# Kernel tuning notes

Measured on AMD Instinct MI355X. Metric: run time of the kernel, lower is better.

The kernel has to match this reference:

```python
import jax, jax.numpy as jnp
import numpy as np
import math

NEG_INF = -1e9
ALPHA = 1.0


def setup_inputs() -> dict:
    key = jax.random.key(0)
    B, T, S, C = 32, 1024, 512, 384
    k1, k2 = jax.random.split(key)
    epsilon = jax.random.normal(k1, (B, T, C), dtype=jnp.float32)
    conditional_inputs = jax.random.normal(k2, (B, S, C), dtype=jnp.float32)
    targets_lengths = jnp.full((B,), T, dtype=jnp.int32)
    condition_lengths = jnp.full((B,), S, dtype=jnp.int32)
    return {
        "epsilon": epsilon,
        "conditional_inputs": conditional_inputs,
        "targets_lengths": targets_lengths,
        "condition_lengths": condition_lengths,
    }


def _forward_dp(E):
    """Log-partition forward DP. E = alpha*Wr, [B,T,S].
    mu[t,j] = E[t,j] + logaddexp(mu[t-1,j], mu[t-1,j-1]); path starts at (0,0)."""
    B, T, S = E.shape
    start = jnp.where(jnp.arange(S) == 0, 0.0, NEG_INF)
    init = E[:, 0, :] + start[None, :]

    def step(mu_prev, e_t):
        shifted = jnp.concatenate([jnp.full((B, 1), NEG_INF, mu_prev.dtype), mu_prev[:, :-1]], axis=1)
        mu_t = e_t + jnp.logaddexp(mu_prev, shifted)
        return mu_t, mu_t

    _, mus = jax.lax.scan(step, init, jnp.moveaxis(E[:, 1:], 1, 0))
    return jnp.concatenate([init[:, None], jnp.moveaxis(mus, 0, 1)], axis=1)  # [B,T,S]


def _backward_dp(E):
    """Backward messages. beta[T-1,j] = 0 at j=S-1 else -inf;
    beta[t,j] = logaddexp(beta[t+1,j]+E[t+1,j], beta[t+1,j+1]+E[t+1,j+1])."""
    B, T, S = E.shape
    init = jnp.broadcast_to(jnp.where(jnp.arange(S) == S - 1, 0.0, NEG_INF), (B, S))

    def step(b_next, e_next):
        m = b_next + e_next
        shifted = jnp.concatenate([m[:, 1:], jnp.full((B, 1), NEG_INF, m.dtype)], axis=1)
        b_t = jnp.logaddexp(m, shifted)
        return b_t, b_t

    _, bs = jax.lax.scan(step, init, jnp.moveaxis(E[:, 1:], 1, 0), reverse=True)
    return jnp.concatenate([jnp.moveaxis(bs, 0, 1), init[:, None]], axis=1)  # [B,T,S]


def _maximum_path(logpi):
    """Viterbi over monotonic paths (stay at j or step to j from j-1 each t).
    Returns binary path [B,T,S]."""
    B, T, S = logpi.shape
    start = jnp.where(jnp.arange(S) == 0, 0.0, NEG_INF)
    init = logpi[:, 0, :] + start[None, :]

    def step(v_prev, lp_t):
        shifted = jnp.concatenate([jnp.full((B, 1), NEG_INF, v_prev.dtype), v_prev[:, :-1]], axis=1)
        v_t = lp_t + jnp.maximum(v_prev, shifted)
        move = shifted > v_prev  # True => predecessor is j-1
        return v_t, move

    _, moves = jax.lax.scan(step, init, jnp.moveaxis(logpi[:, 1:], 1, 0))  # [T-1,B,S]

    j_last = jnp.full((B,), S - 1, dtype=jnp.int32)

    def back(j, move_t):
        came = jnp.take_along_axis(move_t, j[:, None].astype(jnp.int32), axis=1)[:, 0]
        j_prev = j - came.astype(jnp.int32)
        return j_prev, j

    j0, js = jax.lax.scan(back, j_last, moves, reverse=True)  # js[i] = j at time i+1
    js_all = jnp.concatenate([j0[None], js], axis=0)  # [T,B]
    return jax.nn.one_hot(jnp.moveaxis(js_all, 0, 1), S, dtype=logpi.dtype)  # [B,T,S]


def reference(epsilon, conditional_inputs, targets_lengths, condition_lengths):
    B, T, C = epsilon.shape
    S = conditional_inputs.shape[1]
    # initial gaussian sample log-prob, masked by target lengths
    logp_eps = -0.5 * (epsilon ** 2 + math.log(2.0 * math.pi))
    tmask = (jnp.arange(T)[None, :] < targets_lengths[:, None]).astype(epsilon.dtype)
    logprobs = jnp.sum(tmask[:, :, None] * logp_eps, axis=(1, 2))

    z = epsilon  # Glow is external; treated as identity flow (logdet = 0)

    # score matrix + softmax over the target axis (dim 1), as in the source
    Wr = jnp.einsum("btc,bsc->bts", z, conditional_inputs)
    Wr = jax.nn.softmax(Wr, axis=1)

    E = ALPHA * Wr
    mu = _forward_dp(E)
    mu_N = mu[:, -1, -1]
    beta = _backward_dp(E)
    logpi = mu + beta - mu_N[:, None, None]  # posterior node log-marginals

    path = _maximum_path(logpi)  # [B,T,S] binary alignment
    sample_logprob = ALPHA * jnp.sum(path * Wr, axis=(1, 2)) - mu_N
    logprobs = logprobs + sample_logprob
    return path, logprobs
```

## Files before the change

### kernel.cpp

```cpp
#include <hip/hip_runtime.h>
#include <cstdint>
#include <cstddef>

#define B_ 32
#define T_ 1024
#define S_ 512
#define C_ 384
#define HALF_LOG_2PI 0.91893853320467274178f
#define LN2F 0.69314718055994530942f
#define INV_LN2F 1.44269504088896340736f

typedef unsigned short u16;
typedef unsigned long long u64;
typedef __attribute__((ext_vector_type(8))) short bf16x8;
typedef __attribute__((ext_vector_type(4))) float f32x4;

__device__ __forceinline__ unsigned rne16(float f) {
    unsigned b = __float_as_uint(f);
    return (b + 0x7FFFu + ((b >> 16) & 1u)) >> 16;
}
__device__ __forceinline__ uint4 pack8f(float a0, float a1, float a2, float a3,
                                        float a4, float a5, float a6, float a7) {
    uint4 q;
    q.x = rne16(a0) | (rne16(a1) << 16);
    q.y = rne16(a2) | (rne16(a3) << 16);
    q.z = rne16(a4) | (rne16(a5) << 16);
    q.w = rne16(a6) | (rne16(a7) << 16);
    return q;
}
#define UNPK(q, p)                                                              \
    float p##0 = __uint_as_float((q).x << 16),                                  \
          p##1 = __uint_as_float((q).x & 0xFFFF0000u),                          \
          p##2 = __uint_as_float((q).y << 16),                                  \
          p##3 = __uint_as_float((q).y & 0xFFFF0000u),                          \
          p##4 = __uint_as_float((q).z << 16),                                  \
          p##5 = __uint_as_float((q).z & 0xFFFF0000u),                          \
          p##6 = __uint_as_float((q).w << 16),                                  \
          p##7 = __uint_as_float((q).w & 0xFFFF0000u)

#define PROW(t) (*(const uint4*)(Pb  + (size_t)(t) * S_ + l8))
#define BROW(t) (*(const uint4*)(Btb + (size_t)(t) * S_ + l8))

template <int CTRL>
__device__ __forceinline__ float fdpp0(float x) {
    return __uint_as_float((unsigned)__builtin_amdgcn_update_dpp(
        0, (int)__float_as_uint(x), CTRL, 0xF, 0xF, true));
}
__device__ __forceinline__ float wave_fmax(float x) {
    x = fmaxf(x, fdpp0<0x121>(x));
    x = fmaxf(x, fdpp0<0x122>(x));
    x = fmaxf(x, fdpp0<0x124>(x));
    x = fmaxf(x, fdpp0<0x128>(x));
    float a = __uint_as_float((unsigned)__builtin_amdgcn_readlane((int)__float_as_uint(x), 0));
    float b = __uint_as_float((unsigned)__builtin_amdgcn_readlane((int)__float_as_uint(x), 16));
    float c = __uint_as_float((unsigned)__builtin_amdgcn_readlane((int)__float_as_uint(x), 32));
    float d = __uint_as_float((unsigned)__builtin_amdgcn_readlane((int)__float_as_uint(x), 48));
    return fmaxf(fmaxf(a, b), fmaxf(c, d));
}

__device__ __forceinline__ void gll16(const u16* g, u16* l) {
    __builtin_amdgcn_global_load_lds(
        (const __attribute__((address_space(1))) void*)g,
        (__attribute__((address_space(3))) void*)l, 16, 0, 0);
}
#define WAITV(N) do { asm volatile("s_waitcnt vmcnt(" #N ")" ::: "memory");     \
                      __builtin_amdgcn_sched_barrier(0); } while (0)
#define FENCE_LGKM() do { asm volatile("s_waitcnt lgkmcnt(0)" ::: "memory");    \
                          __builtin_amdgcn_sched_barrier(0); } while (0)

__global__ __launch_bounds__(256) void k_pre(const float* __restrict__ eps,
                                             const float* __restrict__ cond,
                                             const int* __restrict__ tlen,
                                             float* __restrict__ lp_part,
                                             u16* __restrict__ Abf,
                                             u16* __restrict__ Bbf) {
    if (blockIdx.x < 1536) {
        const int b = blockIdx.x / 48, chunk = blockIdx.x % 48;
        const int len = tlen[b];
        const float* base = eps + (size_t)b * T_ * C_ + (size_t)chunk * 8192;
        u16* obase = Abf + (size_t)b * T_ * C_ + (size_t)chunk * 8192;
        float acc = 0.f;
        for (int g = threadIdx.x; g < 1024; g += 256) {
            float4 v0 = *(const float4*)(base + g * 8);
            float4 v1 = *(const float4*)(base + g * 8 + 4);
            int t = (chunk * 8192 + g * 8) / C_;
            if (t < len)
                acc += v0.x*v0.x + v0.y*v0.y + v0.z*v0.z + v0.w*v0.w
                     + v1.x*v1.x + v1.y*v1.y + v1.z*v1.z + v1.w*v1.w;
            *(uint4*)(obase + g * 8) = pack8f(v0.x, v0.y, v0.z, v0.w,
                                              v1.x, v1.y, v1.z, v1.w);
        }
        __shared__ float red[256];
        red[threadIdx.x] = acc;
        __syncthreads();
        for (int o = 128; o > 0; o >>= 1) {
            if (threadIdx.x < o) red[threadIdx.x] += red[threadIdx.x + o];
            __syncthreads();
        }
        if (threadIdx.x == 0) lp_part[blockIdx.x] = -0.5f * red[0];
    } else {
        const size_t n8 = (size_t)B_ * S_ * C_ / 8;
        for (size_t i = (size_t)(blockIdx.x - 1536) * 256 + threadIdx.x; i < n8;
             i += (size_t)512 * 256) {
            float4 v0 = *(const float4*)(cond + i * 8);
            float4 v1 = *(const float4*)(cond + i * 8 + 4);
            *(uint4*)(Bbf + i * 8) = pack8f(v0.x, v0.y, v0.z, v0.w,
                                            v1.x, v1.y, v1.z, v1.w);
        }
    }
}

__global__ __launch_bounds__(256) void k_gemm(const u16* __restrict__ A,
                                              const u16* __restrict__ Bc,
                                              u16* __restrict__ Wb) {
    __shared__ u16 Al[4096];
    __shared__ u16 Bl[4096];
    const int b  = blockIdx.z;
    const int m0 = blockIdx.y * 128;
    const int n0 = blockIdx.x * 128;
    const int tid = threadIdx.x;
    const int lane = tid & 63, wid = tid >> 6;
    const int wy = wid >> 1, wx = wid & 1;
    const int r15 = lane & 15, kg = lane >> 4;
    const u16* Ab = A  + (size_t)b * T_ * C_;
    const u16* Bb = Bc + (size_t)b * S_ * C_;

    f32x4 acc[4][4];
#pragma unroll
    for (int i = 0; i < 4; ++i)
#pragma unroll
        for (int j = 0; j < 4; ++j) acc[i][j] = (f32x4){0.f, 0.f, 0.f, 0.f};

    const int g1 = tid + 256;
    const int row0 = tid >> 2, o0 = tid & 3;
    const int row1 = g1 >> 2,  o1 = g1 & 3;
    const int wb0 = (row0 * 64 + o0 * 16) ^ (((row0 >> 1) & 7) << 4);
    const int wb1 = (row1 * 64 + o1 * 16) ^ (((row1 >> 1) & 7) << 4);
    const int rswz = ((r15 >> 1) & 7) << 4;

    for (int k0 = 0; k0 < C_; k0 += 32) {
        uint4 a0 = *(const uint4*)(Ab + (size_t)(m0 + row0) * C_ + k0 + o0 * 8);
        uint4 a1 = *(const uint4*)(Ab + (size_t)(m0 + row1) * C_ + k0 + o1 * 8);
        uint4 c0 = *(const uint4*)(Bb + (size_t)(n0 + row0) * C_ + k0 + o0 * 8);
        uint4 c1 = *(const uint4*)(Bb + (size_t)(n0 + row1) * C_ + k0 + o1 * 8);
        __syncthreads();
        *(uint4*)((char*)Al + wb0) = a0;
        *(uint4*)((char*)Al + wb1) = a1;
        *(uint4*)((char*)Bl + wb0) = c0;
        *(uint4*)((char*)Bl + wb1) = c1;
        __syncthreads();
        bf16x8 af[4], bfb[4];
#pragma unroll
        for (int ar = 0; ar < 4; ++ar) {
            int row = wy * 64 + ar * 16 + r15;
            af[ar] = *(const bf16x8*)((const char*)Al + ((row * 64 + kg * 16) ^ rswz));
        }
#pragma unroll
        for (int bc = 0; bc < 4; ++bc) {
            int row = wx * 64 + bc * 16 + r15;
            bfb[bc] = *(const bf16x8*)((const char*)Bl + ((row * 64 + kg * 16) ^ rswz));
        }
#pragma unroll
        for (int ar = 0; ar < 4; ++ar)
#pragma unroll
            for (int bc = 0; bc < 4; ++bc)
                acc[ar][bc] = __builtin_amdgcn_mfma_f32_16x16x32_bf16(
                    af[ar], bfb[bc], acc[ar][bc], 0, 0, 0);
    }
#pragma unroll
    for (int ar = 0; ar < 4; ++ar) {
        int t = m0 + wy * 64 + ar * 16 + kg * 4;
#pragma unroll
        for (int bc = 0; bc < 4; ++bc) {
            int s = n0 + wx * 64 + bc * 16 + r15;
            u16* dst = Wb + ((size_t)b * T_ + t) * S_ + s;
#pragma unroll
            for (int r = 0; r < 4; ++r) dst[(size_t)r * S_] = (u16)rne16(acc[ar][bc][r]);
        }
    }
}

#define COLU(i, xa, xb, xc, xd) do {                                            \
    float nm = fmaxf(fmaxf(fmaxf(m[i], xa), xb), fmaxf(xc, xd));                \
    s[i] = s[i] * __builtin_amdgcn_exp2f((m[i] - nm) * INV_LN2F)                \
         + __builtin_amdgcn_exp2f((xa - nm) * INV_LN2F)                         \
         + __builtin_amdgcn_exp2f((xb - nm) * INV_LN2F)                         \
         + __builtin_amdgcn_exp2f((xc - nm) * INV_LN2F)                         \
         + __builtin_amdgcn_exp2f((xd - nm) * INV_LN2F);                        \
    m[i] = nm;                                                                  \
} while (0)

__global__ __launch_bounds__(256) void k_stats1(const u16* __restrict__ Wb,
                                                float* __restrict__ pmax,
                                                float* __restrict__ psum) {
    __shared__ float smax[4][S_];
    __shared__ float ssum[4][S_];
    const int c = blockIdx.x & 3;
    const int b = blockIdx.x >> 2;
    const int w = threadIdx.x >> 6, l = threadIdx.x & 63;
    const u16* base = Wb + (size_t)b * T_ * S_ + (size_t)(c * 256 + w * 64) * S_ + l * 8;
    float m[8], s[8];
#pragma unroll
    for (int i = 0; i < 8; ++i) { m[i] = -3.0e38f; s[i] = 0.f; }
    for (int t = 0; t < 64; t += 4) {
        uint4 q0 = *(const uint4*)(base + (size_t)(t + 0) * S_);
        uint4 q1 = *(const uint4*)(base + (size_t)(t + 1) * S_);
        uint4 q2 = *(const uint4*)(base + (size_t)(t + 2) * S_);
        uint4 q3 = *(const uint4*)(base + (size_t)(t + 3) * S_);
        UNPK(q0, xa); UNPK(q1, xb); UNPK(q2, xc); UNPK(q3, xd);
        COLU(0, xa0, xb0, xc0, xd0);
        COLU(1, xa1, xb1, xc1, xd1);
        COLU(2, xa2, xb2, xc2, xd2);
        COLU(3, xa3, xb3, xc3, xd3);
        COLU(4, xa4, xb4, xc4, xd4);
        COLU(5, xa5, xb5, xc5, xd5);
        COLU(6, xa6, xb6, xc6, xd6);
        COLU(7, xa7, xb7, xc7, xd7);
    }
#pragma unroll
    for (int i = 0; i < 8; ++i) {
        smax[w][l * 8 + i] = m[i];
        ssum[w][l * 8 + i] = s[i];
    }
    __syncthreads();
    for (int col = threadIdx.x; col < S_; col += 256) {
        float m0 = smax[0][col], m1 = smax[1][col];
        float m2 = smax[2][col], m3 = smax[3][col];
        float nm = fmaxf(fmaxf(m0, m1), fmaxf(m2, m3));
        float ss = ssum[0][col] * __builtin_amdgcn_exp2f((m0 - nm) * INV_LN2F)
                 + ssum[1][col] * __builtin_amdgcn_exp2f((m1 - nm) * INV_LN2F)
                 + ssum[2][col] * __builtin_amdgcn_exp2f((m2 - nm) * INV_LN2F)
                 + ssum[3][col] * __builtin_amdgcn_exp2f((m3 - nm) * INV_LN2F);
        pmax[(size_t)c * B_ * S_ + b * S_ + col] = nm;
        psum[(size_t)c * B_ * S_ + b * S_ + col] = ss;
    }
}

__global__ __launch_bounds__(256) void k_stats2(const float* __restrict__ pmax,
                                                const float* __restrict__ psum,
                                                float* __restrict__ cmax,
                                                float* __restrict__ cinv) {
    const int i = blockIdx.x * 256 + threadIdx.x;
    float m0 = pmax[i], m1 = pmax[(size_t)B_ * S_ + i];
    float m2 = pmax[(size_t)2 * B_ * S_ + i], m3 = pmax[(size_t)3 * B_ * S_ + i];
    float m = fmaxf(fmaxf(m0, m1), fmaxf(m2, m3));
    float s = psum[i] * expf(m0 - m)
            + psum[(size_t)B_ * S_ + i] * expf(m1 - m)
            + psum[(size_t)2 * B_ * S_ + i] * expf(m2 - m)
            + psum[(size_t)3 * B_ * S_ + i] * expf(m3 - m);
    cmax[i] = m;
    cinv[i] = 1.0f / s;
}

__global__ __launch_bounds__(256) void k_pack(const u16* __restrict__ Wb,
                                              const float* __restrict__ cmax,
                                              const float* __restrict__ cinv,
                                              u16* __restrict__ P) {
    const size_t total8 = (size_t)B_ * T_ * S_ / 8;
    for (size_t i = (size_t)blockIdx.x * 256 + threadIdx.x; i < total8;
         i += (size_t)gridDim.x * 256) {
        size_t base = i * 8;
        int s = (int)(base & (S_ - 1));
        int b = (int)(base >> 19);
        uint4 xq = *(const uint4*)(Wb + base);
        UNPK(xq, x);
        float4 mA = *(const float4*)(cmax + (size_t)b * S_ + s);
        float4 mB = *(const float4*)(cmax + (size_t)b * S_ + s + 4);
        float4 iA = *(const float4*)(cinv + (size_t)b * S_ + s);
        float4 iB = *(const float4*)(cinv + (size_t)b * S_ + s + 4);
        float w0 = __builtin_amdgcn_exp2f(fmaf(x0, INV_LN2F, -mA.x * INV_LN2F)) * iA.x;
        float w1 = __builtin_amdgcn_exp2f(fmaf(x1, INV_LN2F, -mA.y * INV_LN2F)) * iA.y;
        float w2 = __builtin_amdgcn_exp2f(fmaf(x2, INV_LN2F, -mA.z * INV_LN2F)) * iA.z;
        float w3 = __builtin_amdgcn_exp2f(fmaf(x3, INV_LN2F, -mA.w * INV_LN2F)) * iA.w;
        float w4 = __builtin_amdgcn_exp2f(fmaf(x4, INV_LN2F, -mB.x * INV_LN2F)) * iB.x;
        float w5 = __builtin_amdgcn_exp2f(fmaf(x5, INV_LN2F, -mB.y * INV_LN2F)) * iB.y;
        float w6 = __builtin_amdgcn_exp2f(fmaf(x6, INV_LN2F, -mB.z * INV_LN2F)) * iB.z;
        float w7 = __builtin_amdgcn_exp2f(fmaf(x7, INV_LN2F, -mB.w * INV_LN2F)) * iB.w;
        float p0 = __builtin_amdgcn_exp2f(fmaf(w0, INV_LN2F, -2.0f));
        float p1 = __builtin_amdgcn_exp2f(fmaf(w1, INV_LN2F, -2.0f));
        float p2 = __builtin_amdgcn_exp2f(fmaf(w2, INV_LN2F, -2.0f));
        float p3 = __builtin_amdgcn_exp2f(fmaf(w3, INV_LN2F, -2.0f));
        float p4 = __builtin_amdgcn_exp2f(fmaf(w4, INV_LN2F, -2.0f));
        float p5 = __builtin_amdgcn_exp2f(fmaf(w5, INV_LN2F, -2.0f));
        float p6 = __builtin_amdgcn_exp2f(fmaf(w6, INV_LN2F, -2.0f));
        float p7 = __builtin_amdgcn_exp2f(fmaf(w7, INV_LN2F, -2.0f));
        *(uint4*)(P + base) = pack8f(p0, p1, p2, p3, p4, p5, p6, p7);
    }
}

#define RENORM_B() do {                                                         \
    float mx_ = wave_fmax(fmaxf(fmaxf(fmaxf(m0,m1),fmaxf(m2,m3)),               \
                                fmaxf(fmaxf(m4,m5),fmaxf(m6,m7))));             \
    int eb_ = (__float_as_int(mx_) >> 23) & 255;                                \
    float sc_ = (eb_ > 0) ? __int_as_float((254 - eb_) << 23) : 1.0f;           \
    m0*=sc_; m1*=sc_; m2*=sc_; m3*=sc_; m4*=sc_; m5*=sc_; m6*=sc_; m7*=sc_;     \
} while (0)

#define BSTEPD(tt, jj) do {                                                     \
    uint4 q_ = *(const uint4*)&Pl[buf][jj][l8];                                 \
    UNPK(q_, eP);                                                               \
    float z0=m0*eP0, z1=m1*eP1, z2=m2*eP2, z3=m3*eP3;                           \
    float z4=m4*eP4, z5=m5*eP5, z6=m6*eP6, z7=m7*eP7;                           \
    float rt = fdpp0<0x130>(z0);                \
    m0=z0+z1; m1=z1+z2; m2=z2+z3; m3=z3+z4;                                     \
    m4=z4+z5; m5=z5+z6; m6=z6+z7; m7=z7+rt;                                     \
    if ((tt) < w0 + 32) {                                                       \
        uint4 st;                                                               \
        asm("v_cvt_pk_bf16_f32 %0, %1, %2" : "=v"(st.x) : "v"(m0), "v"(m1));    \
        asm("v_cvt_pk_bf16_f32 %0, %1, %2" : "=v"(st.y) : "v"(m2), "v"(m3));    \
        asm("v_cvt_pk_bf16_f32 %0, %1, %2" : "=v"(st.z) : "v"(m4), "v"(m5));    \
        asm("v_cvt_pk_bf16_f32 %0, %1, %2" : "=v"(st.w) : "v"(m6), "v"(m7));    \
        *(uint4*)(Bb + (size_t)(tt) * S_ + l8) = st;                            \
    }                                                                           \
} while (0)

__global__ __launch_bounds__(64) void k_beta(const u16* __restrict__ P,
                                             u16* __restrict__ Bt) {
    __shared__ u16 Pl[2][8][S_];
    const int l = threadIdx.x, l8 = l * 8;
    const int xcd = blockIdx.x & 7;
    const int idx = blockIdx.x >> 3;
    const int c = idx & 31;
    const int b = ((idx >> 5) << 3) + xcd;
    const int w0 = c * 32;
    const u16* Pb = P  + (size_t)b * T_ * S_;
    u16*      Bb = Bt + (size_t)b * T_ * S_;
    float m0, m1, m2, m3, m4, m5, m6, m7;
    int te = w0 + 63;
    if (te > 1023) te = 1023;
    if (te == 1023) {
        m0 = m1 = m2 = m3 = m4 = m5 = m6 = 0.f;
        m7 = (l == 63) ? 1.f : 0.f;
        if (1023 < w0 + 32) {
            uint4 st;
            asm("v_cvt_pk_bf16_f32 %0, %1, %2" : "=v"(st.x) : "v"(m0), "v"(m1));
            asm("v_cvt_pk_bf16_f32 %0, %1, %2" : "=v"(st.y) : "v"(m2), "v"(m3));
            asm("v_cvt_pk_bf16_f32 %0, %1, %2" : "=v"(st.z) : "v"(m4), "v"(m5));
            asm("v_cvt_pk_bf16_f32 %0, %1, %2" : "=v"(st.w) : "v"(m6), "v"(m7));
            *(uint4*)(Bb + (size_t)1023 * S_ + l8) = st;
        }
    } else {
        m0 = m1 = m2 = m3 = m4 = m5 = m6 = m7 = 1.f;
    }
    const int cnt = te - w0;
    const int ng = (cnt + 1) >> 3;
#pragma unroll
    for (int r = 0; r < 8; ++r)
        gll16(Pb + (size_t)(te - r) * S_ + l8, &Pl[0][r][0]);
#pragma unroll
    for (int r = 0; r < 8; ++r)
        gll16(Pb + (size_t)(te - 8 - r) * S_ + l8, &Pl[1][r][0]);
    int tt = te - 1;
    int buf = 0;
    for (int g = 0; g < ng - 1; ++g) {
        WAITV(8);
        BSTEPD(tt - 0, 0);  BSTEPD(tt - 1, 1);  BSTEPD(tt - 2, 2);  BSTEPD(tt - 3, 3);
        BSTEPD(tt - 4, 4);  BSTEPD(tt - 5, 5);  BSTEPD(tt - 6, 6);  BSTEPD(tt - 7, 7);
        RENORM_B();
        FENCE_LGKM();
        if (g + 2 < ng) {
            const int bs = te - 8 * (g + 2);
#pragma unroll
            for (int r = 0; r < 8; ++r)
                gll16(Pb + (size_t)(bs - r) * S_ + l8, &Pl[buf][r][0]);
        }
        __builtin_amdgcn_sched_barrier(0);
        buf ^= 1;
        tt -= 8;
    }
    WAITV(0);
    BSTEPD(tt - 0, 0);  BSTEPD(tt - 1, 1);  BSTEPD(tt - 2, 2);  BSTEPD(tt - 3, 3);
    BSTEPD(tt - 4, 4);  BSTEPD(tt - 5, 5);  BSTEPD(tt - 6, 6);
}

#define RENORM_MI() do {                                                        \
    float mx_ = wave_fmax(fmaxf(fmaxf(fmaxf(m0,m1),fmaxf(m2,m3)),               \
                                fmaxf(fmaxf(m4,m5),fmaxf(m6,m7))));             \
    int eb_ = (__float_as_int(mx_) >> 23) & 255;                                \
    float sc_ = (eb_ > 0) ? __int_as_float((254 - eb_) << 23) : 1.0f;           \
    if (eb_ > 0) ioffM += eb_ - 127;                                            \
    m0*=sc_; m1*=sc_; m2*=sc_; m3*=sc_; m4*=sc_; m5*=sc_; m6*=sc_; m7*=sc_;     \
} while (0)

#define RENORM_VR() do {                                                        \
    float mx_ = wave_fmax(fmaxf(fmaxf(fmaxf(v0,v1),fmaxf(v2,v3)),               \
                                fmaxf(fmaxf(v4,v5),fmaxf(v6,v7))));             \
    int eb_ = (__float_as_int(mx_) >> 23) & 255;                                \
    float sc_ = (eb_ > 0) ? __int_as_float((254 - eb_) << 23) : 0.0f;           \
    float ad_ = (eb_ > 0) ? 0.f : 1.f;                                          \
    v0=fmaf(v0,sc_,ad_); v1=fmaf(v1,sc_,ad_); v2=fmaf(v2,sc_,ad_);              \
    v3=fmaf(v3,sc_,ad_); v4=fmaf(v4,sc_,ad_); v5=fmaf(v5,sc_,ad_);              \
    v6=fmaf(v6,sc_,ad_); v7=fmaf(v7,sc_,ad_);                                   \
} while (0)

#define VSTEPD(TT, jj) do {                                                     \
    uint4 qp_ = *(const uint4*)&Pl[buf][jj][l8];                                \
    uint4 qb_ = *(const uint4*)&Bl[buf][jj][l8];                                \
    UNPK(qp_, eP); UNPK(qb_, eB);                                               \
    float lf = fdpp0<0x138>(m7);                 \
    float n0 = eP0*(m0+lf), n1 = eP1*(m1+m0);                                   \
    float n2 = eP2*(m2+m1), n3 = eP3*(m3+m2);                                   \
    float n4 = eP4*(m4+m3), n5 = eP5*(m5+m4);                                   \
    float n6 = eP6*(m6+m5), n7 = eP7*(m7+m6);                                   \
    float vlf = fdpp0<0x138>(v7);                                               \
    if ((TT) >= w0) {                                                           \
        unsigned cc0=(vlf>v0)?1u:0u, cc1=(v0>v1)?2u:0u, cc2=(v1>v2)?4u:0u,      \
                 cc3=(v2>v3)?8u:0u,  cc4=(v3>v4)?16u:0u, cc5=(v4>v5)?32u:0u,    \
                 cc6=(v5>v6)?64u:0u, cc7=(v6>v7)?128u:0u;                       \
        acc |= ((u64)(cc0|cc1|cc2|cc3|cc4|cc5|cc6|cc7)) << (((TT)&7)*8);        \
        if (((TT)&7) == 7) { mrow[((TT)>>3)*64 + l] = acc; acc = 0ULL; }        \
    }                                                                           \
    float w0v=(n0*eB0)*fmaxf(v0,vlf), w1v=(n1*eB1)*fmaxf(v1,v0);                \
    float w2v=(n2*eB2)*fmaxf(v2,v1),  w3v=(n3*eB3)*fmaxf(v3,v2);                \
    float w4v=(n4*eB4)*fmaxf(v4,v3),  w5v=(n5*eB5)*fmaxf(v5,v4);                \
    float w6v=(n6*eB6)*fmaxf(v6,v5),  w7v=(n7*eB7)*fmaxf(v7,v6);                \
    m0=n0;m1=n1;m2=n2;m3=n3;m4=n4;m5=n5;m6=n6;m7=n7;                            \
    v0=w0v;v1=w1v;v2=w2v;v3=w3v;v4=w4v;v5=w5v;v6=w6v;v7=w7v;                    \
    if ((TT) == wexp) { wex = __shfl(m0, 2 * c); wio = ioffM; }                 \
} while (0)

__global__ __launch_bounds__(64) void k_vit(const u16* __restrict__ P,
                                            const u16* __restrict__ Bt,
                                            u64* __restrict__ mbg,
                                            float* __restrict__ elog,
                                            float* __restrict__ wlg) {
    __shared__ u16 Pl[2][8][S_];
    __shared__ u16 Bl[2][8][S_];
    const int l = threadIdx.x, l8 = l * 8;
    const int xcd = blockIdx.x & 7;
    const int idx = blockIdx.x >> 3;
    const int c = idx & 31;
    const int b = ((idx >> 5) << 3) + xcd;
    const int w0 = c * 32, tend = w0 + 31;
    const int t0 = (w0 >= 32) ? (w0 - 32) : 0;
    const int wexp = w0 - 1;
    const u16* Pb  = P  + (size_t)b * T_ * S_;
    const u16* Btb = Bt + (size_t)b * T_ * S_;
    u64* mrow = mbg + (size_t)b * 8192;

    float m0,m1,m2,m3,m4,m5,m6,m7, v0,v1,v2,v3,v4,v5,v6,v7;
    int ioffM = 0;
    float wex = 1.f; int wio = 0;
    {
        uint4 qp = PROW(t0); UNPK(qp, eP);
        uint4 qb = BROW(t0); UNPK(qb, eB);
        if (t0 == 0) {
            m0 = (l == 0) ? eP0 : 0.f;
            m1 = 0.f; m2 = 0.f; m3 = 0.f; m4 = 0.f; m5 = 0.f; m6 = 0.f; m7 = 0.f;
        } else {
            m0 = eP0; m1 = eP1; m2 = eP2; m3 = eP3;
            m4 = eP4; m5 = eP5; m6 = eP6; m7 = eP7;
        }
        v0 = m0*eB0; v1 = m1*eB1; v2 = m2*eB2; v3 = m3*eB3;
        v4 = m4*eB4; v5 = m5*eB5; v6 = m6*eB6; v7 = m7*eB7;
    }
    u64 acc = 0ULL;
    const int cnt = tend - t0;
    const int ng = (cnt + 1) >> 3;
#pragma unroll
    for (int r = 0; r < 8; ++r) {
        gll16(Pb  + (size_t)(t0 + 1 + r) * S_ + l8, &Pl[0][r][0]);
        gll16(Btb + (size_t)(t0 + 1 + r) * S_ + l8, &Bl[0][r][0]);
    }
#pragma unroll
    for (int r = 0; r < 8; ++r) {
        gll16(Pb  + (size_t)(t0 + 9 + r) * S_ + l8, &Pl[1][r][0]);
        gll16(Btb + (size_t)(t0 + 9 + r) * S_ + l8, &Bl[1][r][0]);
    }
    int t = t0 + 1;
    int buf = 0;
    for (int g = 0; g < ng - 1; ++g) {
        WAITV(16);
        VSTEPD(t + 0, 0);  VSTEPD(t + 1, 1);  VSTEPD(t + 2, 2);  VSTEPD(t + 3, 3);
        VSTEPD(t + 4, 4);  VSTEPD(t + 5, 5);  VSTEPD(t + 6, 6);  VSTEPD(t + 7, 7);
        RENORM_MI();
        RENORM_VR();
        FENCE_LGKM();
        if (g + 2 < ng) {
            const int bs = t0 + 1 + 8 * (g + 2);
#pragma unroll
            for (int r = 0; r < 8; ++r) {
                gll16(Pb  + (size_t)(bs + r) * S_ + l8, &Pl[buf][r][0]);
                gll16(Btb + (size_t)(bs + r) * S_ + l8, &Bl[buf][r][0]);
            }
        }
        __builtin_amdgcn_sched_barrier(0);
        buf ^= 1;
        t += 8;
    }
    WAITV(0);
    VSTEPD(t + 0, 0);  VSTEPD(t + 1, 1);  VSTEPD(t + 2, 2);  VSTEPD(t + 3, 3);
    VSTEPD(t + 4, 4);  VSTEPD(t + 5, 5);  VSTEPD(t + 6, 6);

    float eex = (c == 31) ? __shfl(m7, 63) : __shfl(m0, 2 * (c + 1));
    if (l == 0) {
        elog[b * 32 + c] = __builtin_amdgcn_logf(fmaxf(eex, 1e-35f)) + (float)ioffM;
        if (c >= 1)
            wlg[b * 32 + c] = __builtin_amdgcn_logf(fmaxf(wex, 1e-35f)) + (float)wio;
    }
}

__global__ __launch_bounds__(512) void k_map(const u64* __restrict__ mbg,
                                             u16* __restrict__ map) {
    __shared__ u64 mb[4][64];
    const int b = blockIdx.x >> 5, c = blockIdx.x & 31;
    const int tid = threadIdx.x;
    const u64* src = mbg + (size_t)b * 8192 + (size_t)(4 * c) * 64;
    if (tid < 128) ((uint4*)&mb[0][0])[tid] = ((const uint4*)src)[tid];
    __syncthreads();
    int jj = tid;
    const int kmin = (c == 0) ? 1 : 0;
    for (int k = 31; k >= kmin; --k) {
        u64 word = mb[k >> 3][jj >> 3];
        jj -= (int)((word >> ((k & 7) * 8 + (jj & 7))) & 1ULL);
    }
    map[((size_t)b * 32 + c) * 512 + tid] = (u16)jj;
}

__global__ __launch_bounds__(256) void k_btr2(const u64* __restrict__ mbg,
                                              const u16* __restrict__ map,
                                              int* __restrict__ js) {
    __shared__ u64 mb[128][64];
    __shared__ u16 cent[32];
    const int b = blockIdx.x, tid = threadIdx.x;
    const uint4* src = (const uint4*)(mbg + (size_t)b * 8192);
    uint4* dst = (uint4*)&mb[0][0];
    for (int i = tid; i < 4096; i += 256) dst[i] = src[i];
    if (tid == 0) {
        int jj = 511;
        cent[31] = 511;
        for (int c = 31; c >= 1; --c) {
            jj = (int)map[((size_t)b * 32 + c) * 512 + jj];
            cent[c - 1] = (u16)jj;
        }
    }
    __syncthreads();
    if (tid < 32) {
        const int c = tid;
        int jj = (int)cent[c];
        js[b * T_ + 32 * c + 31] = jj;
        const int kmin = (c == 0) ? 1 : 0;
        for (int k = 31; k >= kmin; --k) {
            const int t = 32 * c + k;
            u64 word = mb[t >> 3][jj >> 3];
            jj -= (int)((word >> ((t & 7) * 8 + (jj & 7))) & 1ULL);
            js[b * T_ + t - 1] = jj;
        }
    }
}

__global__ __launch_bounds__(256) void k_out(const int* __restrict__ js,
                                             const u16* __restrict__ P,
                                             const float* __restrict__ lp_part,
                                             const int* __restrict__ tlen,
                                             const float* __restrict__ elog,
                                             const float* __restrict__ wlg,
                                             float* __restrict__ outp,
                                             float* __restrict__ out_lp) {
    if (blockIdx.x < 4096) {
        const size_t total4 = (size_t)B_ * T_ * S_ / 4;
        float4* O = (float4*)outp;
        for (size_t i = (size_t)blockIdx.x * 256 + threadIdx.x; i < total4;
             i += (size_t)4096 * 256) {
            size_t base = i * 4;
            int s = (int)(base & (S_ - 1));
            int row = (int)(base >> 9);
            int jt = js[row];
            float4 o;
            o.x = (s == jt) ? 1.f : 0.f;
            o.y = (s + 1 == jt) ? 1.f : 0.f;
            o.z = (s + 2 == jt) ? 1.f : 0.f;
            o.w = (s + 3 == jt) ? 1.f : 0.f;
            O[i] = o;
        }
    } else {
        const int b = blockIdx.x - 4096;
        float acc = 0.f;
        for (int t = threadIdx.x; t < T_; t += 256) {
            int jt = js[b * T_ + t];
            unsigned u = P[((size_t)b * T_ + t) * S_ + jt];
            acc += __builtin_amdgcn_logf(__uint_as_float(u << 16));
        }
        __shared__ float red[256];
        red[threadIdx.x] = acc;
        __syncthreads();
        for (int o = 128; o > 0; o >>= 1) {
            if (threadIdx.x < o) red[threadIdx.x] += red[threadIdx.x + o];
            __syncthreads();
        }
        if (threadIdx.x == 0) {
            float basep = 0.f;
            for (int i = 0; i < 48; ++i) basep += lp_part[b * 48 + i];
            float mu2n = elog[b * 32 + 31];
            for (int cc = 1; cc < 32; ++cc)
                mu2n += elog[b * 32 + cc - 1] - wlg[b * 32 + cc];
            out_lp[b] = basep - HALF_LOG_2PI * ((float)tlen[b] * C_)
                        + LN2F * (red[0] - mu2n);
        }
    }
}

extern "C" void kernel_launch(void* const* d_in, const int* in_sizes, int n_in,
                              void* d_out, int out_size, void* d_ws, size_t ws_size,
                              hipStream_t stream) {
    const float* eps  = (const float*)d_in[0];
    const float* cond = (const float*)d_in[1];
    const int* tlen   = (const int*)d_in[2];

    float* out_path = (float*)d_out;
    float* out_lp   = out_path + (size_t)B_ * T_ * S_;

    const size_t NBTS = (size_t)B_ * T_ * S_;
    char* w = (char*)d_ws;
    u16*   Wb   = (u16*)w;
    u16*   P    = Wb + NBTS;
    u16*   Bt   = P + NBTS;
    u16*   Abf  = Bt + NBTS;
    u16*   Bbf  = Abf + (size_t)B_ * T_ * C_;
    u64*   mbg  = (u64*)(Bbf + (size_t)B_ * S_ * C_);
    float* pmax = (float*)(mbg + (size_t)B_ * 8192);
    float* psum = pmax + (size_t)4 * B_ * S_;
    float* cmax = psum + (size_t)4 * B_ * S_;
    float* cinv = cmax + (size_t)B_ * S_;
    float* lp_part = cinv + (size_t)B_ * S_;
    float* elog = lp_part + B_ * 48;
    float* wlg  = elog + B_ * 32;
    int*   js   = (int*)(wlg + B_ * 32);
    u16*   map  = (u16*)(js + B_ * T_);

    k_pre<<<2048, 256, 0, stream>>>(eps, cond, tlen, lp_part, Abf, Bbf);
    k_gemm<<<dim3(S_ / 128, T_ / 128, B_), 256, 0, stream>>>(Abf, Bbf, Wb);
    k_stats1<<<B_ * 4, 256, 0, stream>>>(Wb, pmax, psum);
    k_stats2<<<B_ * S_ / 256, 256, 0, stream>>>(pmax, psum, cmax, cinv);
    k_pack<<<2048, 256, 0, stream>>>(Wb, cmax, cinv, P);
    k_beta<<<B_ * 32, 64, 0, stream>>>(P, Bt);
    k_vit<<<B_ * 32, 64, 0, stream>>>(P, Bt, mbg, elog, wlg);
    k_map<<<B_ * 32, 512, 0, stream>>>(mbg, map);
    k_btr2<<<B_, 256, 0, stream>>>(mbg, map, js);
    k_out<<<4096 + B_, 256, 0, stream>>>(js, P, lp_part, tlen, elog, wlg,
                                         out_path, out_lp);
}
```

Baseline: 158.9 us.

## Fuse bf16 conversion into GEMM loads and deepen beta/viterbi prefetch pipeline

Result: slower. 180.1 us (+13.3%).

```diff
diff --git a/kernel.cpp b/kernel.cpp
--- a/kernel.cpp
+++ b/kernel.cpp
@@ -18,6 +18,14 @@
 __device__ __forceinline__ unsigned rne16(float f) {
     unsigned b = __float_as_uint(f);
     return (b + 0x7FFFu + ((b >> 16) & 1u)) >> 16;
+}
+__device__ __forceinline__ uint4 cvt8(float4 lo, float4 hi) {
+    uint4 q;
+    asm("v_cvt_pk_bf16_f32 %0, %1, %2" : "=v"(q.x) : "v"(lo.x), "v"(lo.y));
+    asm("v_cvt_pk_bf16_f32 %0, %1, %2" : "=v"(q.y) : "v"(lo.z), "v"(lo.w));
+    asm("v_cvt_pk_bf16_f32 %0, %1, %2" : "=v"(q.z) : "v"(hi.x), "v"(hi.y));
+    asm("v_cvt_pk_bf16_f32 %0, %1, %2" : "=v"(q.w) : "v"(hi.z), "v"(hi.w));
+    return q;
 }
 __device__ __forceinline__ uint4 pack8f(float a0, float a1, float a2, float a3,
                                         float a4, float a5, float a6, float a7) {
@@ -68,50 +76,33 @@
 #define FENCE_LGKM() do { asm volatile("s_waitcnt lgkmcnt(0)" ::: "memory");    \
                           __builtin_amdgcn_sched_barrier(0); } while (0)
 
-__global__ __launch_bounds__(256) void k_pre(const float* __restrict__ eps,
-                                             const float* __restrict__ cond,
+__global__ __launch_bounds__(256) void k_eps(const float* __restrict__ eps,
                                              const int* __restrict__ tlen,
-                                             float* __restrict__ lp_part,
-                                             u16* __restrict__ Abf,
-                                             u16* __restrict__ Bbf) {
-    if (blockIdx.x < 1536) {
-        const int b = blockIdx.x / 48, chunk = blockIdx.x % 48;
-        const int len = tlen[b];
-        const float* base = eps + (size_t)b * T_ * C_ + (size_t)chunk * 8192;
-        u16* obase = Abf + (size_t)b * T_ * C_ + (size_t)chunk * 8192;
-        float acc = 0.f;
-        for (int g = threadIdx.x; g < 1024; g += 256) {
-            float4 v0 = *(const float4*)(base + g * 8);
-            float4 v1 = *(const float4*)(base + g * 8 + 4);
-            int t = (chunk * 8192 + g * 8) / C_;
-            if (t < len)
-                acc += v0.x*v0.x + v0.y*v0.y + v0.z*v0.z + v0.w*v0.w
-                     + v1.x*v1.x + v1.y*v1.y + v1.z*v1.z + v1.w*v1.w;
-            *(uint4*)(obase + g * 8) = pack8f(v0.x, v0.y, v0.z, v0.w,
-                                              v1.x, v1.y, v1.z, v1.w);
-        }
-        __shared__ float red[256];
-        red[threadIdx.x] = acc;
+                                             float* __restrict__ lp_part) {
+    const int b = blockIdx.x / 48, chunk = blockIdx.x % 48;
+    const int len = tlen[b];
+    const float* base = eps + (size_t)b * T_ * C_ + (size_t)chunk * 8192;
+    float acc = 0.f;
+    for (int g = threadIdx.x; g < 1024; g += 256) {
+        float4 v0 = *(const float4*)(base + g * 8);
+        float4 v1 = *(const float4*)(base + g * 8 + 4);
+        int t = (chunk * 8192 + g * 8) / C_;
+        if (t < len)
+            acc += v0.x*v0.x + v0.y*v0.y + v0.z*v0.z + v0.w*v0.w
+                 + v1.x*v1.x + v1.y*v1.y + v1.z*v1.z + v1.w*v1.w;
+    }
+    __shared__ float red[256];
+    red[threadIdx.x] = acc;
+    __syncthreads();
+    for (int o = 128; o > 0; o >>= 1) {
+        if (threadIdx.x < o) red[threadIdx.x] += red[threadIdx.x + o];
         __syncthreads();
-        for (int o = 128; o > 0; o >>= 1) {
-            if (threadIdx.x < o) red[threadIdx.x] += red[threadIdx.x + o];
-            __syncthreads();
-        }
-        if (threadIdx.x == 0) lp_part[blockIdx.x] = -0.5f * red[0];
-    } else {
-        const size_t n8 = (size_t)B_ * S_ * C_ / 8;
-        for (size_t i = (size_t)(blockIdx.x - 1536) * 256 + threadIdx.x; i < n8;
-             i += (size_t)512 * 256) {
-            float4 v0 = *(const float4*)(cond + i * 8);
-            float4 v1 = *(const float4*)(cond + i * 8 + 4);
-            *(uint4*)(Bbf + i * 8) = pack8f(v0.x, v0.y, v0.z, v0.w,
-                                            v1.x, v1.y, v1.z, v1.w);
-        }
-    }
-}
-
-__global__ __launch_bounds__(256) void k_gemm(const u16* __restrict__ A,
-                                              const u16* __restrict__ Bc,
+    }
+    if (threadIdx.x == 0) lp_part[blockIdx.x] = -0.5f * red[0];
+}
+
+__global__ __launch_bounds__(256) void k_gemm(const float* __restrict__ A,
+                                              const float* __restrict__ Bc,
                                               u16* __restrict__ Wb) {
     __shared__ u16 Al[4096];
     __shared__ u16 Bl[4096];
@@ -122,8 +113,8 @@
     const int lane = tid & 63, wid = tid >> 6;
     const int wy = wid >> 1, wx = wid & 1;
     const int r15 = lane & 15, kg = lane >> 4;
-    const u16* Ab = A  + (size_t)b * T_ * C_;
-    const u16* Bb = Bc + (size_t)b * S_ * C_;
+    const float* Ab = A  + (size_t)b * T_ * C_;
+    const float* Bb = Bc + (size_t)b * S_ * C_;
 
     f32x4 acc[4][4];
 #pragma unroll
@@ -131,18 +122,23 @@
 #pragma unroll
         for (int j = 0; j < 4; ++j) acc[i][j] = (f32x4){0.f, 0.f, 0.f, 0.f};
 
-    const int g1 = tid + 256;
     const int row0 = tid >> 2, o0 = tid & 3;
-    const int row1 = g1 >> 2,  o1 = g1 & 3;
+    const int row1 = row0 + 64;
     const int wb0 = (row0 * 64 + o0 * 16) ^ (((row0 >> 1) & 7) << 4);
-    const int wb1 = (row1 * 64 + o1 * 16) ^ (((row1 >> 1) & 7) << 4);
+    const int wb1 = (row1 * 64 + o0 * 16) ^ (((row1 >> 1) & 7) << 4);
     const int rswz = ((r15 >> 1) & 7) << 4;
 
     for (int k0 = 0; k0 < C_; k0 += 32) {
-        uint4 a0 = *(const uint4*)(Ab + (size_t)(m0 + row0) * C_ + k0 + o0 * 8);
-        uint4 a1 = *(const uint4*)(Ab + (size_t)(m0 + row1) * C_ + k0 + o1 * 8);
-        uint4 c0 = *(const uint4*)(Bb + (size_t)(n0 + row0) * C_ + k0 + o0 * 8);
-        uint4 c1 = *(const uint4*)(Bb + (size_t)(n0 + row1) * C_ + k0 + o1 * 8);
+        const float* pa0 = Ab + (size_t)(m0 + row0) * C_ + k0 + o0 * 8;
+        const float* pa1 = Ab + (size_t)(m0 + row1) * C_ + k0 + o0 * 8;
+        const float* pc0 = Bb + (size_t)(n0 + row0) * C_ + k0 + o0 * 8;
+        const float* pc1 = Bb + (size_t)(n0 + row1) * C_ + k0 + o0 * 8;
+        float4 aL0 = *(const float4*)pa0, aH0 = *(const float4*)(pa0 + 4);
+        float4 aL1 = *(const float4*)pa1, aH1 = *(const float4*)(pa1 + 4);
+        float4 cL0 = *(const float4*)pc0, cH0 = *(const float4*)(pc0 + 4);
+        float4 cL1 = *(const float4*)pc1, cH1 = *(const float4*)(pc1 + 4);
+        uint4 a0 = cvt8(aL0, aH0), a1 = cvt8(aL1, aH1);
+        uint4 c0 = cvt8(cL0, cH0), c1 = cvt8(cL1, cH1);
         __syncthreads();
         *(uint4*)((char*)Al + wb0) = a0;
         *(uint4*)((char*)Al + wb1) = a1;
@@ -314,9 +310,16 @@
     }                                                                           \
 } while (0)
 
+#define BISSUE(g) do {                                                          \
+    const int bs_ = te - 8 * (g);                                               \
+    _Pragma("unroll")                                                           \
+    for (int r = 0; r < 8; ++r)                                                 \
+        gll16(Pb + (size_t)(bs_ - r) * S_ + l8, &Pl[(g) & 3][r][0]);            \
+} while (0)
+
 __global__ __launch_bounds__(64) void k_beta(const u16* __restrict__ P,
                                              u16* __restrict__ Bt) {
-    __shared__ u16 Pl[2][8][S_];
+    __shared__ u16 Pl[4][8][S_];
     const int l = threadIdx.x, l8 = l * 8;
     const int xcd = blockIdx.x & 7;
     const int idx = blockIdx.x >> 3;
@@ -344,28 +347,20 @@
     }
     const int cnt = te - w0;
     const int ng = (cnt + 1) >> 3;
-#pragma unroll
-    for (int r = 0; r < 8; ++r)
-        gll16(Pb + (size_t)(te - r) * S_ + l8, &Pl[0][r][0]);
-#pragma unroll
-    for (int r = 0; r < 8; ++r)
-        gll16(Pb + (size_t)(te - 8 - r) * S_ + l8, &Pl[1][r][0]);
+    BISSUE(0);
+    BISSUE(1);
+    BISSUE(2);
     int tt = te - 1;
     int buf = 0;
     for (int g = 0; g < ng - 1; ++g) {
-        WAITV(8);
+        WAITV(16);
         BSTEPD(tt - 0, 0);  BSTEPD(tt - 1, 1);  BSTEPD(tt - 2, 2);  BSTEPD(tt - 3, 3);
         BSTEPD(tt - 4, 4);  BSTEPD(tt - 5, 5);  BSTEPD(tt - 6, 6);  BSTEPD(tt - 7, 7);
         RENORM_B();
         FENCE_LGKM();
-        if (g + 2 < ng) {
-            const int bs = te - 8 * (g + 2);
-#pragma unroll
-            for (int r = 0; r < 8; ++r)
-                gll16(Pb + (size_t)(bs - r) * S_ + l8, &Pl[buf][r][0]);
-        }
+        if (g + 3 < ng) BISSUE(g + 3);
         __builtin_amdgcn_sched_barrier(0);
-        buf ^= 1;
+        buf = (buf + 1) & 3;
         tt -= 8;
     }
     WAITV(0);
@@ -394,8 +389,8 @@
 } while (0)
 
 #define VSTEPD(TT, jj) do {                                                     \
-    uint4 qp_ = *(const uint4*)&Pl[buf][jj][l8];                                \
-    uint4 qb_ = *(const uint4*)&Bl[buf][jj][l8];                                \
+    uint4 qp_ = *(const uint4*)&Pl[buf][jj][l8];                                 \
+    uint4 qb_ = *(const uint4*)&Bl[buf][jj][l8];                                 \
     UNPK(qp_, eP); UNPK(qb_, eB);                                               \
     float lf = fdpp0<0x138>(m7);                 \
     float n0 = eP0*(m0+lf), n1 = eP1*(m1+m0);                                   \
@@ -419,13 +414,22 @@
     if ((TT) == wexp) { wex = __shfl(m0, 2 * c); wio = ioffM; }                 \
 } while (0)
 
+#define VISSUE(g) do {                                                          \
+    const int bs_ = t0 + 1 + 8 * (g);                                           \
+    _Pragma("unroll")                                                           \
+    for (int r = 0; r < 8; ++r) {                                               \
+        gll16(Pb  + (size_t)(bs_ + r) * S_ + l8, &Pl[(g) & 3][r][0]);           \
+        gll16(Btb + (size_t)(bs_ + r) * S_ + l8, &Bl[(g) & 3][r][0]);           \
+    }                                                                           \
+} while (0)
+
 __global__ __launch_bounds__(64) void k_vit(const u16* __restrict__ P,
                                             const u16* __restrict__ Bt,
                                             u64* __restrict__ mbg,
                                             float* __restrict__ elog,
                                             float* __restrict__ wlg) {
-    __shared__ u16 Pl[2][8][S_];
-    __shared__ u16 Bl[2][8][S_];
+    __shared__ u16 Pl[4][8][S_];
+    __shared__ u16 Bl[4][8][S_];
     const int l = threadIdx.x, l8 = l * 8;
     const int xcd = blockIdx.x & 7;
     const int idx = blockIdx.x >> 3;
@@ -457,35 +461,21 @@
     u64 acc = 0ULL;
     const int cnt = tend - t0;
     const int ng = (cnt + 1) >> 3;
-#pragma unroll
-    for (int r = 0; r < 8; ++r) {
-        gll16(Pb  + (size_t)(t0 + 1 + r) * S_ + l8, &Pl[0][r][0]);
-        gll16(Btb + (size_t)(t0 + 1 + r) * S_ + l8, &Bl[0][r][0]);
-    }
-#pragma unroll
-    for (int r = 0; r < 8; ++r) {
-        gll16(Pb  + (size_t)(t0 + 9 + r) * S_ + l8, &Pl[1][r][0]);
-        gll16(Btb + (size_t)(t0 + 9 + r) * S_ + l8, &Bl[1][r][0]);
-    }
+    VISSUE(0);
+    VISSUE(1);
+    VISSUE(2);
     int t = t0 + 1;
     int buf = 0;
     for (int g = 0; g < ng - 1; ++g) {
-        WAITV(16);
+        WAITV(32);
         VSTEPD(t + 0, 0);  VSTEPD(t + 1, 1);  VSTEPD(t + 2, 2);  VSTEPD(t + 3, 3);
         VSTEPD(t + 4, 4);  VSTEPD(t + 5, 5);  VSTEPD(t + 6, 6);  VSTEPD(t + 7, 7);
         RENORM_MI();
         RENORM_VR();
         FENCE_LGKM();
-        if (g + 2 < ng) {
-            const int bs = t0 + 1 + 8 * (g + 2);
-#pragma unroll
-            for (int r = 0; r < 8; ++r) {
-                gll16(Pb  + (size_t)(bs + r) * S_ + l8, &Pl[buf][r][0]);
-                gll16(Btb + (size_t)(bs + r) * S_ + l8, &Bl[buf][r][0]);
-            }
-        }
+        if (g + 3 < ng) VISSUE(g + 3);
         __builtin_amdgcn_sched_barrier(0);
-        buf ^= 1;
+        buf = (buf + 1) & 3;
         t += 8;
     }
     WAITV(0);
@@ -615,9 +605,7 @@
     u16*   Wb   = (u16*)w;
     u16*   P    = Wb + NBTS;
     u16*   Bt   = P + NBTS;
-    u16*   Abf  = Bt + NBTS;
-    u16*   Bbf  = Abf + (size_t)B_ * T_ * C_;
-    u64*   mbg  = (u64*)(Bbf + (size_t)B_ * S_ * C_);
+    u64*   mbg  = (u64*)(Bt + NBTS);
     float* pmax = (float*)(mbg + (size_t)B_ * 8192);
     float* psum = pmax + (size_t)4 * B_ * S_;
     float* cmax = psum + (size_t)4 * B_ * S_;
@@ -628,8 +616,8 @@
     int*   js   = (int*)(wlg + B_ * 32);
     u16*   map  = (u16*)(js + B_ * T_);
 
-    k_pre<<<2048, 256, 0, stream>>>(eps, cond, tlen, lp_part, Abf, Bbf);
-    k_gemm<<<dim3(S_ / 128, T_ / 128, B_), 256, 0, stream>>>(Abf, Bbf, Wb);
+    k_eps<<<B_ * 48, 256, 0, stream>>>(eps, tlen, lp_part);
+    k_gemm<<<dim3(S_ / 128, T_ / 128, B_), 256, 0, stream>>>(eps, cond, Wb);
     k_stats1<<<B_ * 4, 256, 0, stream>>>(Wb, pmax, psum);
     k_stats2<<<B_ * S_ / 256, 256, 0, stream>>>(pmax, psum, cmax, cinv);
     k_pack<<<2048, 256, 0, stream>>>(Wb, cmax, cinv, P);
```
